# Optimization experiments

Measured on AMD Instinct MI355X. Metric: run time of the kernel, lower is better.

## Reference

```python
import jax, jax.numpy as jnp
import numpy as np

B, T, D = 2, 2048, 1024
NH, NKV, HD = 16, 4, 64
ROPE = 16  # partial RoPE dims (first 16 of 64)
HALF = ROPE // 2


def apply_rope(x, cos, sin):
    # x: (B, nH, T, HD); rotate first ROPE dims, pass the rest through
    x1 = x[..., :HALF]
    x2 = x[..., HALF:ROPE]
    xp = x[..., ROPE:]
    c = cos[None, None, :, :]  # (1,1,T,HALF)
    s = sin[None, None, :, :]
    return jnp.concatenate([x1 * c - x2 * s, x1 * s + x2 * c, xp], axis=-1)


def setup_inputs() -> dict:
    key = jax.random.key(0)
    k0, k1, k2 = jax.random.split(key, 3)
    x = jax.random.normal(k0, (B, T, D), dtype=jnp.float32)
    # RoPE tables for the rotated sub-dimension (half = ROPE//2 = 8)
    inv_freq = 1.0 / (10000.0 ** (jnp.arange(HALF, dtype=jnp.float32) / HALF))
    ang = jnp.arange(T, dtype=jnp.float32)[:, None] * inv_freq[None, :]
    cos = jnp.cos(ang)
    sin = jnp.sin(ang)
    attn_mask = jnp.tril(jnp.ones((T, T), dtype=bool))  # causal
    w_qkv = jax.random.normal(k1, ((NH + 2 * NKV) * HD, D), dtype=jnp.float32) * (D ** -0.5)
    w_out = jax.random.normal(k2, (D, D), dtype=jnp.float32) * (D ** -0.5)
    q_scale = jnp.full((NH, 1), 1.5, dtype=jnp.float32)
    k_scale = jnp.full((NKV, 1), 1.5, dtype=jnp.float32)
    return {"x": x, "cos": cos, "sin": sin, "attn_mask": attn_mask,
            "w_qkv": w_qkv, "w_out": w_out, "q_scale": q_scale, "k_scale": k_scale}


def reference(x, cos, sin, attn_mask, w_qkv, w_out, q_scale, k_scale):
    Bx, Tx, C = x.shape
    groups = NH // NKV
    qkv = x @ w_qkv.T  # (B,T,(NH+2*NKV)*HD)
    q, k, v = jnp.split(qkv, [NH * HD, (NH + NKV) * HD], axis=-1)
    q = q.reshape(Bx, Tx, NH, HD).transpose(0, 2, 1, 3)    # (B,NH,T,HD)
    k = k.reshape(Bx, Tx, NKV, HD).transpose(0, 2, 1, 3)   # (B,NKV,T,HD)
    v = v.reshape(Bx, Tx, NKV, HD).transpose(0, 2, 1, 3)
    # per-head qk gain scaling
    q = q * q_scale[None, :, :, None]  # (1,NH,1,1)
    k = k * k_scale[None, :, :, None]
    # partial RoPE on q and k
    q = apply_rope(q, cos[:Tx], sin[:Tx])
    k = apply_rope(k, cos[:Tx], sin[:Tx])
    # GQA expand (repeat_interleave along heads)
    ke = jnp.repeat(k, groups, axis=1)  # (B,NH,T,HD)
    ve = jnp.repeat(v, groups, axis=1)
    # scaled dot-product attention with causal mask
    scores = jnp.einsum('bhqd,bhkd->bhqk', q, ke) * (HD ** -0.5)
    scores = jnp.where(attn_mask[None, None], scores, -jnp.inf)
    probs = jax.nn.softmax(scores, axis=-1)
    ao = jnp.einsum('bhqk,bhkd->bhqd', probs, ve)  # (B,NH,T,HD)
    # xsa: subtract self-component along the (shared) kv value direction
    ao_r = ao.reshape(Bx, NKV, groups, Tx, HD)
    vv = v[:, :, None]  # (B,NKV,1,T,HD), broadcasts over groups
    dots = jnp.sum(ao_r * vv, axis=-1, keepdims=True)
    norm = jnp.maximum(jnp.sum(vv * vv, axis=-1, keepdims=True), 1e-8)
    ao = (ao_r - (dots / norm) * vv).reshape(Bx, NH, Tx, HD)
    out = ao.transpose(0, 2, 1, 3).reshape(Bx, Tx, C) @ w_out.T
    return out
```

## Files before the change

### kernel.cpp

```cpp
#include <hip/hip_runtime.h>
#include <hip/hip_bf16.h>

#define NB 2
#define NT 2048
#define ND 1024
#define NHEADS 16
#define NKVH 4
#define HDIM 64
#define QKVD 1536

typedef __attribute__((ext_vector_type(8))) short short8;
typedef __attribute__((ext_vector_type(4))) float floatx4;

__device__ __forceinline__ unsigned short f2bf(float f) {
  union { float f; unsigned int u; } cv; cv.f = f;
  unsigned int u = cv.u;
  u += 0x7fffu + ((u >> 16) & 1u);
  return (unsigned short)(u >> 16);
}
__device__ __forceinline__ float bf2f(unsigned short u) {
  union { unsigned int u; float f; } cv; cv.u = ((unsigned int)u) << 16; return cv.f;
}

__global__ __launch_bounds__(256) void cvt_bf16(const float* __restrict__ in,
                                                unsigned short* __restrict__ out,
                                                int n4) {
  int i = blockIdx.x * 256 + threadIdx.x;
  if (i < n4) {
    float4 v = ((const float4*)in)[i];
    ushort4 o;
    o.x = f2bf(v.x); o.y = f2bf(v.y); o.z = f2bf(v.z); o.w = f2bf(v.w);
    ((ushort4*)out)[i] = o;
  }
}

__global__ __launch_bounds__(256) void gemm12864(
    const unsigned short* __restrict__ A,
    const unsigned short* __restrict__ Bm,
    float* __restrict__ C, int M, int N, int K)
{
  __shared__ __align__(16) short As[128][40];
  __shared__ __align__(16) short Bs[64][40];

  const int tid  = threadIdx.x;
  const int wid  = tid >> 6;
  const int lane = tid & 63;
  const int quad = lane >> 4;
  const int l16  = lane & 15;
  const int wm = wid * 32;
  const int m0 = blockIdx.x * 128;
  const int n0 = blockIdx.y * 64;

  const int r0 = tid >> 2, c0 = (tid & 3) * 8;
  const unsigned short* ag0 = A  + (size_t)(m0 + r0) * K + c0;
  const unsigned short* ag1 = ag0 + (size_t)64 * K;
  const unsigned short* bg0 = Bm + (size_t)(n0 + r0) * K + c0;

  floatx4 acc[2][4] = {};

  for (int k0 = 0; k0 < K; k0 += 32) {
    short8 a0 = *(const short8*)(ag0 + k0);
    short8 a1 = *(const short8*)(ag1 + k0);
    short8 b0 = *(const short8*)(bg0 + k0);
    *(short8*)&As[r0][c0]      = a0;
    *(short8*)&As[r0 + 64][c0] = a1;
    *(short8*)&Bs[r0][c0]      = b0;
    __syncthreads();

    short8 af[2], bf[4];
#pragma unroll
    for (int mi = 0; mi < 2; mi++) af[mi] = *(const short8*)&As[wm + mi * 16 + l16][quad * 8];
#pragma unroll
    for (int ni = 0; ni < 4; ni++) bf[ni] = *(const short8*)&Bs[ni * 16 + l16][quad * 8];
#pragma unroll
    for (int mi = 0; mi < 2; mi++)
#pragma unroll
      for (int ni = 0; ni < 4; ni++)
        acc[mi][ni] = __builtin_amdgcn_mfma_f32_16x16x32_bf16(af[mi], bf[ni], acc[mi][ni], 0, 0, 0);
    __syncthreads();
  }

#pragma unroll
  for (int mi = 0; mi < 2; mi++)
#pragma unroll
    for (int ni = 0; ni < 4; ni++)
#pragma unroll
      for (int r = 0; r < 4; r++) {
        int m = m0 + wm + mi * 16 + quad * 4 + r;
        int n = n0 + ni * 16 + l16;
        C[(size_t)m * N + n] = acc[mi][ni][r];
      }
}

__global__ __launch_bounds__(256) void rope_pack(
    const float* __restrict__ qkv,
    const float* __restrict__ cosT, const float* __restrict__ sinT,
    const float* __restrict__ q_scale, const float* __restrict__ k_scale,
    unsigned short* __restrict__ qb, unsigned short* __restrict__ kb)
{
  const int b  = blockIdx.z;
  const int hh = blockIdx.y * 4 + (threadIdx.x >> 6);
  const int d  = threadIdx.x & 63;

  float scale; int soff; unsigned short* dbase;
  if (hh < NHEADS) {
    scale = q_scale[hh] * (0.125f * 1.44269504088896f);
    soff = hh * HDIM;
    dbase = qb + ((size_t)(b * NHEADS + hh) * NT) * HDIM;
  } else {
    int kvh = hh - NHEADS;
    scale = k_scale[kvh];
    soff = NHEADS * HDIM + kvh * HDIM;
    dbase = kb + ((size_t)(b * NKVH + kvh) * NT) * HDIM;
  }

  for (int i = 0; i < 8; i++) {
    const int t = blockIdx.x * 8 + i;
    const float* src = qkv + ((size_t)(b * NT + t)) * QKVD + soff;
    float out;
    if (d < 8) {
      float x1 = src[d], x2 = src[d + 8];
      float c = cosT[t * 8 + d], s = sinT[t * 8 + d];
      out = (x1 * c - x2 * s) * scale;
    } else if (d < 16) {
      float x1 = src[d - 8], x2 = src[d];
      float c = cosT[t * 8 + d - 8], s = sinT[t * 8 + d - 8];
      out = (x1 * s + x2 * c) * scale;
    } else {
      out = src[d] * scale;
    }
    dbase[(size_t)t * HDIM + d] = f2bf(out);
  }
}

__global__ __launch_bounds__(256) void vT(const float* __restrict__ qkv,
                                          unsigned short* __restrict__ vtb)
{
  const int tt  = blockIdx.x;
  const int kvh = blockIdx.y;
  const int b   = blockIdx.z;
  const int tid = threadIdx.x;

  __shared__ float tile[64][65];

  {
    const int tl = tid >> 2, d0 = (tid & 3) * 16;
    const float* src = qkv + ((size_t)(b * NT + tt * 64 + tl)) * QKVD
                       + (NHEADS + NKVH) * HDIM + kvh * HDIM + d0;
#pragma unroll
    for (int j = 0; j < 16; j += 4) {
      float4 v = *(const float4*)(src + j);
      tile[tl][d0 + j + 0] = v.x; tile[tl][d0 + j + 1] = v.y;
      tile[tl][d0 + j + 2] = v.z; tile[tl][d0 + j + 3] = v.w;
    }
  }
  __syncthreads();
  {
    const int dd = tid >> 2, t0 = (tid & 3) * 16;
    unsigned short* dst = vtb + ((size_t)((b * NKVH + kvh) * HDIM + dd)) * NT + tt * 64 + t0;
#pragma unroll
    for (int j = 0; j < 16; j++) dst[j] = f2bf(tile[t0 + j][dd]);
  }
}

__global__ __launch_bounds__(256) void fattn(
    const unsigned short* __restrict__ qb,
    const unsigned short* __restrict__ kb,
    const unsigned short* __restrict__ vtb,
    unsigned short* __restrict__ aob,
    float* __restrict__ pbuf)
{
  const int idx = blockIdx.x;
  const int h = blockIdx.y, b = blockIdx.z;
  const int kv = h >> 2;

  int qt, j0, cnt, chunk; bool direct;
  if (idx < 16) { qt = 16 + idx; j0 = 0; cnt = 16; chunk = 0; direct = false; }
  else {
    int rel = idx - 16, s = 16 - (rel >> 1);
    if ((rel & 1) == 0) { qt = s - 1;  j0 = 0;  cnt = s; chunk = 0; direct = true;  }
    else                { qt = s + 15; j0 = 16; cnt = s; chunk = 1; direct = false; }
  }

  const int tid = threadIdx.x;
  const int wid = tid >> 6, lane = tid & 63;
  const int quad = lane >> 4, l16 = lane & 15;
  const int hi8 = l16 >> 3, lo8 = l16 & 7;

  __shared__ __align__(16) short Ks[64][64];
  __shared__ __align__(16) short Vs[64][64];
  __shared__ __align__(16) short Ps[4][16][64];

  const unsigned short* qg = qb + ((size_t)((b * NHEADS + h) * NT + qt * 64)) * HDIM;
  const int qrow = wid * 16 + l16;
  short8 aq0 = *(const short8*)(qg + (size_t)qrow * HDIM + quad * 8);
  short8 aq1 = *(const short8*)(qg + (size_t)qrow * HDIM + 32 + quad * 8);

  const int sr0 = tid >> 3,          sc0 = tid & 7;
  const int sr1 = (tid + 256) >> 3,  sc1 = (tid + 256) & 7;
  short* kst0 = &Ks[sr0][(sc0 ^ (sr0 & 7)) * 8];
  short* kst1 = &Ks[sr1][(sc1 ^ (sr1 & 7)) * 8];
  short* vst0 = &Vs[sr0][(sc0 ^ (sr0 & 7)) * 8];
  short* vst1 = &Vs[sr1][(sc1 ^ (sr1 & 7)) * 8];
  const unsigned short* kgp0 = kb + ((size_t)((b * NKVH + kv) * NT) + sr0) * HDIM + sc0 * 8;
  const unsigned short* kgp1 = kb + ((size_t)((b * NKVH + kv) * NT) + sr1) * HDIM + sc1 * 8;
  const unsigned short* vgp0 = vtb + ((size_t)((b * NKVH + kv) * HDIM) + sr0) * NT + sc0 * 8;
  const unsigned short* vgp1 = vtb + ((size_t)((b * NKVH + kv) * HDIM) + sr1) * NT + sc1 * 8;

  const int cs0 = (quad ^ lo8) * 8;
  const int cs1 = cs0 ^ 32;

  int pwo[4][4];
#pragma unroll
  for (int r = 0; r < 4; r++) {
    const int row = quad * 4 + r;
#pragma unroll
    for (int nb = 0; nb < 4; nb++)
      pwo[r][nb] = wid * 1024 + row * 64 + (((nb * 2 + hi8) ^ (row & 7)) * 8) + lo8;
  }
  short* psf = &Ps[0][0][0];

  floatx4 acc_o[4] = {};
  float lsum[4] = {0.f, 0.f, 0.f, 0.f};

  short8 pk0 = *(const short8*)(kgp0 + (size_t)j0 * 64 * HDIM);
  short8 pk1 = *(const short8*)(kgp1 + (size_t)j0 * 64 * HDIM);
  short8 pv0 = *(const short8*)(vgp0 + j0 * 64);
  short8 pv1 = *(const short8*)(vgp1 + j0 * 64);

  for (int i = 0; i < cnt; i++) {
    const int jt = j0 + i;
    *(short8*)kst0 = pk0;
    *(short8*)kst1 = pk1;
    *(short8*)vst0 = pv0;
    *(short8*)vst1 = pv1;
    __syncthreads();

    if (i + 1 < cnt) {
      pk0 = *(const short8*)(kgp0 + (size_t)(jt + 1) * 64 * HDIM);
      pk1 = *(const short8*)(kgp1 + (size_t)(jt + 1) * 64 * HDIM);
      pv0 = *(const short8*)(vgp0 + (jt + 1) * 64);
      pv1 = *(const short8*)(vgp1 + (jt + 1) * 64);
    }

    floatx4 s[4] = {};
#pragma unroll
    for (int nb = 0; nb < 4; nb++) {
      short8 bk0 = *(const short8*)&Ks[nb * 16 + l16][cs0];
      short8 bk1 = *(const short8*)&Ks[nb * 16 + l16][cs1];
      s[nb] = __builtin_amdgcn_mfma_f32_16x16x32_bf16(aq0, bk0, s[nb], 0, 0, 0);
      s[nb] = __builtin_amdgcn_mfma_f32_16x16x32_bf16(aq1, bk1, s[nb], 0, 0, 0);
    }

    if (jt == qt) {
#pragma unroll
      for (int nb = 0; nb < 4; nb++) {
        int col = nb * 16 + l16;
#pragma unroll
        for (int r = 0; r < 4; r++)
          if (col > wid * 16 + quad * 4 + r) s[nb][r] = -INFINITY;
      }
    }

#pragma unroll
    for (int r = 0; r < 4; r++) {
#pragma unroll
      for (int nb = 0; nb < 4; nb++) {
        float p = __builtin_amdgcn_exp2f(s[nb][r]);
        lsum[r] += p;
        psf[pwo[r][nb]] = (short)f2bf(p);
      }
    }

    short8 ap0 = *(const short8*)&Ps[wid][l16][cs0];
    short8 ap1 = *(const short8*)&Ps[wid][l16][cs1];
#pragma unroll
    for (int nb = 0; nb < 4; nb++) {
      short8 bv0 = *(const short8*)&Vs[nb * 16 + l16][cs0];
      short8 bv1 = *(const short8*)&Vs[nb * 16 + l16][cs1];
      acc_o[nb] = __builtin_amdgcn_mfma_f32_16x16x32_bf16(ap0, bv0, acc_o[nb], 0, 0, 0);
      acc_o[nb] = __builtin_amdgcn_mfma_f32_16x16x32_bf16(ap1, bv1, acc_o[nb], 0, 0, 0);
    }
    __syncthreads();
  }

  if (direct) {
#pragma unroll
    for (int r = 0; r < 4; r++) {
      float ls = lsum[r];
#pragma unroll
      for (int off = 1; off < 16; off <<= 1) ls += __shfl_xor(ls, off);
      const float invl = 1.f / ls;

      const int rowl = wid * 16 + quad * 4 + r;
      const int vcol = ((rowl >> 3) ^ lo8) * 8 + (rowl & 7);
      float vd[4], dot = 0.f, vv = 0.f;
#pragma unroll
      for (int nb = 0; nb < 4; nb++) {
        vd[nb] = bf2f((unsigned short)Vs[nb * 16 + l16][vcol]);
        dot += acc_o[nb][r] * invl * vd[nb];
        vv  += vd[nb] * vd[nb];
      }
#pragma unroll
      for (int off = 1; off < 16; off <<= 1) {
        dot += __shfl_xor(dot, off);
        vv  += __shfl_xor(vv, off);
      }
      const float coef = dot / fmaxf(vv, 1e-8f);
      unsigned short* dst = aob + ((size_t)(b * NT + qt * 64 + rowl)) * ND + h * HDIM + l16;
#pragma unroll
      for (int nb = 0; nb < 4; nb++)
        dst[nb * 16] = f2bf(acc_o[nb][r] * invl - coef * vd[nb]);
    }
  } else {
    const int slot = ((b * NHEADS + h) * 16 + (qt - 16)) * 2 + chunk;
    float* pO = pbuf + (size_t)slot * 4160;
    float* pl = pO + 4096;
#pragma unroll
    for (int r = 0; r < 4; r++) {
      float ls = lsum[r];
#pragma unroll
      for (int off = 1; off < 16; off <<= 1) ls += __shfl_xor(ls, off);
      const int rowl = wid * 16 + quad * 4 + r;
      if (l16 == 0) pl[rowl] = ls;
#pragma unroll
      for (int nb = 0; nb < 4; nb++)
        pO[rowl * 64 + nb * 16 + l16] = acc_o[nb][r];
    }
  }
}

__global__ __launch_bounds__(256) void redn(
    const float* __restrict__ pbuf,
    const unsigned short* __restrict__ vtb,
    unsigned short* __restrict__ aob)
{
  const int qt = 16 + blockIdx.x;
  const int h = blockIdx.y, b = blockIdx.z;
  const int kv = h >> 2;
  const int tid = threadIdx.x;

  const int slot0 = ((b * NHEADS + h) * 16 + blockIdx.x) * 2;
  const float* O0 = pbuf + (size_t)slot0 * 4160;
  const float* O1 = O0 + 4160;
  const float* l0 = O0 + 4096;
  const float* l1 = O1 + 4096;

  __shared__ short vt[64][66];

  {
    const int d = tid >> 2, tq = (tid & 3) * 16;
    const unsigned short* src = vtb + ((size_t)((b * NKVH + kv) * HDIM + d)) * NT + qt * 64 + tq;
    short8 v0 = *(const short8*)src;
    short8 v1 = *(const short8*)(src + 8);
    *(short8*)&vt[d][tq] = v0;
    *(short8*)&vt[d][tq + 8] = v1;
  }
  __syncthreads();

  const int row = tid >> 2, dq = tid & 3;
  const float invl = 1.f / (l0[row] + l1[row]);

  float o[16], vd[16];
  float dot = 0.f, vv = 0.f;
#pragma unroll
  for (int j = 0; j < 16; j++) {
    const int d = dq * 16 + j;
    float ov = (O0[row * 64 + d] + O1[row * 64 + d]) * invl;
    float v  = bf2f((unsigned short)vt[d][row]);
    o[j] = ov; vd[j] = v;
    dot += ov * v; vv += v * v;
  }
  dot += __shfl_xor(dot, 1); dot += __shfl_xor(dot, 2);
  vv  += __shfl_xor(vv, 1);  vv  += __shfl_xor(vv, 2);
  const float coef = dot / fmaxf(vv, 1e-8f);

  unsigned short* dst = aob + ((size_t)(b * NT + qt * 64 + row)) * ND + h * HDIM + dq * 16;
  ushort4 w0, w1, w2, w3;
  w0.x = f2bf(o[0] - coef * vd[0]);  w0.y = f2bf(o[1] - coef * vd[1]);
  w0.z = f2bf(o[2] - coef * vd[2]);  w0.w = f2bf(o[3] - coef * vd[3]);
  w1.x = f2bf(o[4] - coef * vd[4]);  w1.y = f2bf(o[5] - coef * vd[5]);
  w1.z = f2bf(o[6] - coef * vd[6]);  w1.w = f2bf(o[7] - coef * vd[7]);
  w2.x = f2bf(o[8] - coef * vd[8]);  w2.y = f2bf(o[9] - coef * vd[9]);
  w2.z = f2bf(o[10] - coef * vd[10]); w2.w = f2bf(o[11] - coef * vd[11]);
  w3.x = f2bf(o[12] - coef * vd[12]); w3.y = f2bf(o[13] - coef * vd[13]);
  w3.z = f2bf(o[14] - coef * vd[14]); w3.w = f2bf(o[15] - coef * vd[15]);
  ((ushort4*)dst)[0] = w0; ((ushort4*)dst)[1] = w1;
  ((ushort4*)dst)[2] = w2; ((ushort4*)dst)[3] = w3;
}

extern "C" void kernel_launch(void* const* d_in, const int* in_sizes, int n_in,
                              void* d_out, int out_size, void* d_ws, size_t ws_size,
                              hipStream_t stream) {
  const float* x       = (const float*)d_in[0];
  const float* cosT    = (const float*)d_in[1];
  const float* sinT    = (const float*)d_in[2];
  const float* w_qkv   = (const float*)d_in[4];
  const float* w_out   = (const float*)d_in[5];
  const float* q_scale = (const float*)d_in[6];
  const float* k_scale = (const float*)d_in[7];
  float* out = (float*)d_out;

  char* ws = (char*)d_ws;
  unsigned short* xb    = (unsigned short*)ws;
  unsigned short* qb    = xb;
  unsigned short* wqkvb = (unsigned short*)(ws + 8388608);
  unsigned short* kb    = wqkvb;
  unsigned short* woutb = (unsigned short*)(ws + 11534336);
  float*          qkv   = (float*)(ws + 13631488);
  float*          pbuf  = qkv;
  unsigned short* vtb   = (unsigned short*)(ws + 38797312);
  unsigned short* aob   = (unsigned short*)(ws + 40894464);

  cvt_bf16<<<(NB * NT * ND / 4 + 255) / 256, 256, 0, stream>>>(x, xb, NB * NT * ND / 4);
  cvt_bf16<<<(QKVD * ND / 4 + 255) / 256, 256, 0, stream>>>(w_qkv, wqkvb, QKVD * ND / 4);
  cvt_bf16<<<(ND * ND / 4 + 255) / 256, 256, 0, stream>>>(w_out, woutb, ND * ND / 4);

  gemm12864<<<dim3(NB * NT / 128, QKVD / 64), 256, 0, stream>>>(
      xb, wqkvb, qkv, NB * NT, QKVD, ND);

  rope_pack<<<dim3(NT / 8, 5, NB), 256, 0, stream>>>(qkv, cosT, sinT, q_scale, k_scale, qb, kb);
  vT<<<dim3(NT / 64, NKVH, NB), 256, 0, stream>>>(qkv, vtb);

  fattn<<<dim3(48, NHEADS, NB), 256, 0, stream>>>(qb, kb, vtb, aob, pbuf);
  redn<<<dim3(16, NHEADS, NB), 256, 0, stream>>>(pbuf, vtb, aob);

  gemm12864<<<dim3(NB * NT / 128, ND / 64), 256, 0, stream>>>(
      aob, woutb, out, NB * NT, ND, ND);
}
```

Measured before the change: 220.1 us.

## Double-buffer GEMM and attention tiles with direct global-to-LDS loads

Both projection GEMMs move to a 128x128 tile with 4x4 MFMA fragments per wave and a double-buffered LDS stage, loaded through the global_load_lds builtin with an XOR swizzle. The attention kernel double-buffers its K/V tiles the same way and drops the trailing barrier, aiming to overlap the next tile's loads with the current compute and skip the register round trip. The P-to-bf16 conversion now truncates instead of rounding. This adds risk around wait and barrier ordering for the async LDS loads, gives fewer GEMM blocks, and slightly changes numerics.

```diff
diff --git a/kernel.cpp b/kernel.cpp
--- a/kernel.cpp
+++ b/kernel.cpp
@@ -11,6 +11,26 @@
 
 typedef __attribute__((ext_vector_type(8))) short short8;
 typedef __attribute__((ext_vector_type(4))) float floatx4;
+
+#if defined(__has_builtin)
+#  if __has_builtin(__builtin_amdgcn_global_load_lds)
+#    define HAS_GLL 1
+#  endif
+#endif
+#ifndef HAS_GLL
+#  define HAS_GLL 0
+#endif
+
+__device__ __forceinline__ void gll16(const void* g, void* l, int lane) {
+#if HAS_GLL
+  (void)lane;
+  __builtin_amdgcn_global_load_lds(
+      (const __attribute__((address_space(1))) unsigned int*)g,
+      (__attribute__((address_space(3))) unsigned int*)l, 16, 0, 0);
+#else
+  *(short8*)((short*)l) = *(const short8*)g;
+#endif
+}
 
 __device__ __forceinline__ unsigned short f2bf(float f) {
   union { float f; unsigned int u; } cv; cv.f = f;
@@ -34,60 +54,73 @@
   }
 }
 
-__global__ __launch_bounds__(256) void gemm12864(
+__global__ __launch_bounds__(256) void gemm_lds(
     const unsigned short* __restrict__ A,
     const unsigned short* __restrict__ Bm,
     float* __restrict__ C, int M, int N, int K)
 {
-  __shared__ __align__(16) short As[128][40];
-  __shared__ __align__(16) short Bs[64][40];
-
-  const int tid  = threadIdx.x;
-  const int wid  = tid >> 6;
-  const int lane = tid & 63;
-  const int quad = lane >> 4;
-  const int l16  = lane & 15;
-  const int wm = wid * 32;
-  const int m0 = blockIdx.x * 128;
-  const int n0 = blockIdx.y * 64;
-
-  const int r0 = tid >> 2, c0 = (tid & 3) * 8;
-  const unsigned short* ag0 = A  + (size_t)(m0 + r0) * K + c0;
+  __shared__ __align__(16) short As[2][128][32];
+  __shared__ __align__(16) short Bs[2][128][32];
+
+  const int tid = threadIdx.x;
+  const int wid = tid >> 6, lane = tid & 63;
+  const int quad = lane >> 4, l16 = lane & 15;
+  const int wm = (wid >> 1) * 64, wn = (wid & 1) * 64;
+  const int m0 = blockIdx.x * 128, n0 = blockIdx.y * 128;
+
+  const int r0 = tid >> 2;
+  const int lc = ((tid & 3) ^ (r0 & 3)) * 8;
+
+  const unsigned short* ag0 = A  + (size_t)(m0 + r0) * K + lc;
   const unsigned short* ag1 = ag0 + (size_t)64 * K;
-  const unsigned short* bg0 = Bm + (size_t)(n0 + r0) * K + c0;
-
-  floatx4 acc[2][4] = {};
-
-  for (int k0 = 0; k0 < K; k0 += 32) {
-    short8 a0 = *(const short8*)(ag0 + k0);
-    short8 a1 = *(const short8*)(ag1 + k0);
-    short8 b0 = *(const short8*)(bg0 + k0);
-    *(short8*)&As[r0][c0]      = a0;
-    *(short8*)&As[r0 + 64][c0] = a1;
-    *(short8*)&Bs[r0][c0]      = b0;
+  const unsigned short* bg0 = Bm + (size_t)(n0 + r0) * K + lc;
+  const unsigned short* bg1 = bg0 + (size_t)64 * K;
+
+  short* asb = &As[0][0][0];
+  short* bsb = &Bs[0][0][0];
+  const int lofs = (HAS_GLL ? wid * 512 : tid * 8);
+
+  const int cs = (quad ^ (l16 & 3)) * 8;
+
+  floatx4 acc[4][4] = {};
+
+  gll16(ag0, asb + lofs, lane);
+  gll16(ag1, asb + 2048 + lofs, lane);
+  gll16(bg0, bsb + lofs, lane);
+  gll16(bg1, bsb + 2048 + lofs, lane);
+
+  const int NIT = K / 32;
+  for (int it = 0; it < NIT; it++) {
     __syncthreads();
-
-    short8 af[2], bf[4];
-#pragma unroll
-    for (int mi = 0; mi < 2; mi++) af[mi] = *(const short8*)&As[wm + mi * 16 + l16][quad * 8];
-#pragma unroll
-    for (int ni = 0; ni < 4; ni++) bf[ni] = *(const short8*)&Bs[ni * 16 + l16][quad * 8];
-#pragma unroll
-    for (int mi = 0; mi < 2; mi++)
+    const int bi = it & 1, bn = bi ^ 1;
+    if (it + 1 < NIT) {
+      const int k = (it + 1) * 32;
+      gll16(ag0 + k, asb + bn * 4096 + lofs, lane);
+      gll16(ag1 + k, asb + bn * 4096 + 2048 + lofs, lane);
+      gll16(bg0 + k, bsb + bn * 4096 + lofs, lane);
+      gll16(bg1 + k, bsb + bn * 4096 + 2048 + lofs, lane);
+    }
+
+    short8 af[4], bf[4];
+#pragma unroll
+    for (int mi = 0; mi < 4; mi++) af[mi] = *(const short8*)&As[bi][wm + mi * 16 + l16][cs];
+#pragma unroll
+    for (int ni = 0; ni < 4; ni++) bf[ni] = *(const short8*)&Bs[bi][wn + ni * 16 + l16][cs];
+#pragma unroll
+    for (int mi = 0; mi < 4; mi++)
 #pragma unroll
       for (int ni = 0; ni < 4; ni++)
         acc[mi][ni] = __builtin_amdgcn_mfma_f32_16x16x32_bf16(af[mi], bf[ni], acc[mi][ni], 0, 0, 0);
-    __syncthreads();
-  }
-
-#pragma unroll
-  for (int mi = 0; mi < 2; mi++)
+  }
+
+#pragma unroll
+  for (int mi = 0; mi < 4; mi++)
 #pragma unroll
     for (int ni = 0; ni < 4; ni++)
 #pragma unroll
       for (int r = 0; r < 4; r++) {
         int m = m0 + wm + mi * 16 + quad * 4 + r;
-        int n = n0 + ni * 16 + l16;
+        int n = n0 + wn + ni * 16 + l16;
         C[(size_t)m * N + n] = acc[mi][ni][r];
       }
 }
@@ -187,8 +220,8 @@
   const int quad = lane >> 4, l16 = lane & 15;
   const int hi8 = l16 >> 3, lo8 = l16 & 7;
 
-  __shared__ __align__(16) short Ks[64][64];
-  __shared__ __align__(16) short Vs[64][64];
+  __shared__ __align__(16) short Ks[2][64][64];
+  __shared__ __align__(16) short Vs[2][64][64];
   __shared__ __align__(16) short Ps[4][16][64];
 
   const unsigned short* qg = qb + ((size_t)((b * NHEADS + h) * NT + qt * 64)) * HDIM;
@@ -196,16 +229,13 @@
   short8 aq0 = *(const short8*)(qg + (size_t)qrow * HDIM + quad * 8);
   short8 aq1 = *(const short8*)(qg + (size_t)qrow * HDIM + 32 + quad * 8);
 
-  const int sr0 = tid >> 3,          sc0 = tid & 7;
-  const int sr1 = (tid + 256) >> 3,  sc1 = (tid + 256) & 7;
-  short* kst0 = &Ks[sr0][(sc0 ^ (sr0 & 7)) * 8];
-  short* kst1 = &Ks[sr1][(sc1 ^ (sr1 & 7)) * 8];
-  short* vst0 = &Vs[sr0][(sc0 ^ (sr0 & 7)) * 8];
-  short* vst1 = &Vs[sr1][(sc1 ^ (sr1 & 7)) * 8];
-  const unsigned short* kgp0 = kb + ((size_t)((b * NKVH + kv) * NT) + sr0) * HDIM + sc0 * 8;
-  const unsigned short* kgp1 = kb + ((size_t)((b * NKVH + kv) * NT) + sr1) * HDIM + sc1 * 8;
-  const unsigned short* vgp0 = vtb + ((size_t)((b * NKVH + kv) * HDIM) + sr0) * NT + sc0 * 8;
-  const unsigned short* vgp1 = vtb + ((size_t)((b * NKVH + kv) * HDIM) + sr1) * NT + sc1 * 8;
+  const int sr  = tid >> 3;
+  const int lck = ((tid & 7) ^ (sr & 7)) * 8;
+  const unsigned short* kgp0 = kb  + ((size_t)((b * NKVH + kv) * NT) + sr) * HDIM + lck;
+  const unsigned short* vgp0 = vtb + ((size_t)((b * NKVH + kv) * HDIM) + sr) * NT + lck;
+  short* ksb = &Ks[0][0][0];
+  short* vsb = &Vs[0][0][0];
+  const int lofs = (HAS_GLL ? wid * 512 : tid * 8);
 
   const int cs0 = (quad ^ lo8) * 8;
   const int cs1 = cs0 ^ 32;
@@ -223,31 +253,33 @@
   floatx4 acc_o[4] = {};
   float lsum[4] = {0.f, 0.f, 0.f, 0.f};
 
-  short8 pk0 = *(const short8*)(kgp0 + (size_t)j0 * 64 * HDIM);
-  short8 pk1 = *(const short8*)(kgp1 + (size_t)j0 * 64 * HDIM);
-  short8 pv0 = *(const short8*)(vgp0 + j0 * 64);
-  short8 pv1 = *(const short8*)(vgp1 + j0 * 64);
+  {
+    const unsigned short* kg = kgp0 + (size_t)j0 * 64 * HDIM;
+    const unsigned short* vg = vgp0 + j0 * 64;
+    gll16(kg, ksb + lofs, lane);
+    gll16(kg + 32 * HDIM, ksb + 2048 + lofs, lane);
+    gll16(vg, vsb + lofs, lane);
+    gll16(vg + (size_t)32 * NT, vsb + 2048 + lofs, lane);
+  }
 
   for (int i = 0; i < cnt; i++) {
     const int jt = j0 + i;
-    *(short8*)kst0 = pk0;
-    *(short8*)kst1 = pk1;
-    *(short8*)vst0 = pv0;
-    *(short8*)vst1 = pv1;
     __syncthreads();
-
+    const int bi = i & 1, bn = bi ^ 1;
     if (i + 1 < cnt) {
-      pk0 = *(const short8*)(kgp0 + (size_t)(jt + 1) * 64 * HDIM);
-      pk1 = *(const short8*)(kgp1 + (size_t)(jt + 1) * 64 * HDIM);
-      pv0 = *(const short8*)(vgp0 + (jt + 1) * 64);
-      pv1 = *(const short8*)(vgp1 + (jt + 1) * 64);
+      const unsigned short* kg = kgp0 + (size_t)(jt + 1) * 64 * HDIM;
+      const unsigned short* vg = vgp0 + (jt + 1) * 64;
+      gll16(kg, ksb + bn * 4096 + lofs, lane);
+      gll16(kg + 32 * HDIM, ksb + bn * 4096 + 2048 + lofs, lane);
+      gll16(vg, vsb + bn * 4096 + lofs, lane);
+      gll16(vg + (size_t)32 * NT, vsb + bn * 4096 + 2048 + lofs, lane);
     }
 
     floatx4 s[4] = {};
 #pragma unroll
     for (int nb = 0; nb < 4; nb++) {
-      short8 bk0 = *(const short8*)&Ks[nb * 16 + l16][cs0];
-      short8 bk1 = *(const short8*)&Ks[nb * 16 + l16][cs1];
+      short8 bk0 = *(const short8*)&Ks[bi][nb * 16 + l16][cs0];
+      short8 bk1 = *(const short8*)&Ks[bi][nb * 16 + l16][cs1];
       s[nb] = __builtin_amdgcn_mfma_f32_16x16x32_bf16(aq0, bk0, s[nb], 0, 0, 0);
       s[nb] = __builtin_amdgcn_mfma_f32_16x16x32_bf16(aq1, bk1, s[nb], 0, 0, 0);
     }
@@ -268,7 +300,7 @@
       for (int nb = 0; nb < 4; nb++) {
         float p = __builtin_amdgcn_exp2f(s[nb][r]);
         lsum[r] += p;
-        psf[pwo[r][nb]] = (short)f2bf(p);
+        psf[pwo[r][nb]] = (short)(__float_as_uint(p) >> 16);
       }
     }
 
@@ -276,13 +308,14 @@
     short8 ap1 = *(const short8*)&Ps[wid][l16][cs1];
 #pragma unroll
     for (int nb = 0; nb < 4; nb++) {
-      short8 bv0 = *(const short8*)&Vs[nb * 16 + l16][cs0];
-      short8 bv1 = *(const short8*)&Vs[nb * 16 + l16][cs1];
+      short8 bv0 = *(const short8*)&Vs[bi][nb * 16 + l16][cs0];
+      short8 bv1 = *(const short8*)&Vs[bi][nb * 16 + l16][cs1];
       acc_o[nb] = __builtin_amdgcn_mfma_f32_16x16x32_bf16(ap0, bv0, acc_o[nb], 0, 0, 0);
       acc_o[nb] = __builtin_amdgcn_mfma_f32_16x16x32_bf16(ap1, bv1, acc_o[nb], 0, 0, 0);
     }
-    __syncthreads();
-  }
+  }
+
+  const int bl = (cnt - 1) & 1;
 
   if (direct) {
 #pragma unroll
@@ -297,7 +330,7 @@
       float vd[4], dot = 0.f, vv = 0.f;
 #pragma unroll
       for (int nb = 0; nb < 4; nb++) {
-        vd[nb] = bf2f((unsigned short)Vs[nb * 16 + l16][vcol]);
+        vd[nb] = bf2f((unsigned short)Vs[bl][nb * 16 + l16][vcol]);
         dot += acc_o[nb][r] * invl * vd[nb];
         vv  += vd[nb] * vd[nb];
       }
@@ -416,7 +449,7 @@
   cvt_bf16<<<(QKVD * ND / 4 + 255) / 256, 256, 0, stream>>>(w_qkv, wqkvb, QKVD * ND / 4);
   cvt_bf16<<<(ND * ND / 4 + 255) / 256, 256, 0, stream>>>(w_out, woutb, ND * ND / 4);
 
-  gemm12864<<<dim3(NB * NT / 128, QKVD / 64), 256, 0, stream>>>(
+  gemm_lds<<<dim3(NB * NT / 128, QKVD / 128), 256, 0, stream>>>(
       xb, wqkvb, qkv, NB * NT, QKVD, ND);
 
   rope_pack<<<dim3(NT / 8, 5, NB), 256, 0, stream>>>(qkv, cosT, sinT, q_scale, k_scale, qb, kb);
@@ -425,6 +458,6 @@
   fattn<<<dim3(48, NHEADS, NB), 256, 0, stream>>>(qb, kb, vtb, aob, pbuf);
   redn<<<dim3(16, NHEADS, NB), 256, 0, stream>>>(pbuf, vtb, aob);
 
-  gemm12864<<<dim3(NB * NT / 128, ND / 64), 256, 0, stream>>>(
+  gemm_lds<<<dim3(NB * NT / 128, ND / 128), 256, 0, stream>>>(
       aob, woutb, out, NB * NT, ND, ND);
 }
```

After: 216.2 us. About the same (-1.8%).
